# Kernel tuning notes

Hardware: AMD Instinct MI355X
Metric: run time of the kernel (lower is better)

The kernel has to match this reference:

```python
import jax, jax.numpy as jnp
import numpy as np

NUM_USER = 20000
NUM_ITEM = 20000
N = NUM_USER + NUM_ITEM
E = 250000
DIM_X = 64
NEG_SLOPE = 0.01  # F.leaky_relu default
EPS = 1e-12


def _xavier(key, shape):
    scale = (2.0 / (shape[0] + shape[1])) ** 0.5
    return jax.random.normal(key, shape, dtype=jnp.float32) * scale


def setup_inputs() -> dict:
    key = jax.random.key(0)
    ks = iter(jax.random.split(key, 64))
    inp = {}
    feat_dims = {'v': 2048, 'a': 128, 't': 100}
    lat_dims = {'v': 256, 'a': 128, 't': 100}
    for m in ('v', 'a', 't'):
        Fd, L = feat_dims[m], lat_dims[m]
        inp[m + '_feat'] = jax.random.normal(next(ks), (NUM_ITEM, Fd), dtype=jnp.float32)
        inp[m + '_pref'] = _xavier(next(ks), (NUM_USER, L))
        inp[m + '_mlp_w'] = _xavier(next(ks), (Fd, L))
        inp[m + '_mlp_b'] = jnp.zeros((L,), jnp.float32)
        inp[m + '_conv_w'] = _xavier(next(ks), (L, L))
        inp[m + '_conv_b'] = jnp.zeros((L,), jnp.float32)
        inp[m + '_lin_w'] = _xavier(next(ks), (L, DIM_X))
        inp[m + '_lin_b'] = jnp.zeros((DIM_X,), jnp.float32)
        inp[m + '_g_w'] = _xavier(next(ks), (L, DIM_X))
        inp[m + '_g_b'] = jnp.zeros((DIM_X,), jnp.float32)
    inp['id_emb'] = _xavier(next(ks), (N, DIM_X))
    src = jax.random.randint(next(ks), (E,), 0, NUM_USER)
    dst = jax.random.randint(next(ks), (E,), NUM_USER, N)
    inp['edge_index'] = jnp.stack([src, dst])  # [2, E] user->item
    inp['user_nodes'] = jax.random.randint(next(ks), (1024,), 0, NUM_USER)
    inp['pos_items'] = jax.random.randint(next(ks), (1024,), NUM_USER, N)
    inp['neg_items'] = jax.random.randint(next(ks), (1024,), NUM_USER, N)
    return inp


def _l2norm(x):
    return x / jnp.maximum(jnp.linalg.norm(x, axis=-1, keepdims=True), EPS)


def _graph_gat(x, src, dst, w, b):
    # x: [N, L] -> per-edge gather, gated attention, scatter-add (aggr='add')
    xw = x @ w                      # [N, L]
    x_j = xw[src]                   # source (neighbor) features, [E, L]
    x_i = xw[dst]                   # destination features, [E, L]
    inner = jnp.sum(x_i * x_j, axis=-1)                      # [E]
    deg = jax.ops.segment_sum(jnp.ones_like(inner), src, num_segments=N)
    gate = jax.nn.sigmoid(inner * (deg[src] ** -0.5))        # degree-scaled gate
    logits = inner * gate
    seg_max = jax.ops.segment_max(logits, dst, num_segments=N)
    e = jnp.exp(logits - seg_max[dst])
    denom = jax.ops.segment_sum(e, dst, num_segments=N)
    alpha = e / jnp.maximum(denom[dst], 1e-16)               # softmax over in-edges of dst
    out = jax.ops.segment_sum(x_j * alpha[:, None], dst, num_segments=N)
    return _l2norm(out + b)


def _gnn(feat, pref, mlp_w, mlp_b, conv_w, conv_b, lin_w, lin_b, g_w, g_b, id_emb, src, dst):
    temp = jnp.tanh(feat @ mlp_w + mlp_b)                    # [num_item, L]
    x = _l2norm(jnp.concatenate([pref, temp], axis=0))        # [N, L]
    h = jax.nn.leaky_relu(_graph_gat(x, src, dst, conv_w, conv_b), NEG_SLOPE)
    x_hat = jax.nn.leaky_relu(x @ lin_w + lin_b, NEG_SLOPE) + id_emb
    return jax.nn.leaky_relu(h @ g_w + g_b + x_hat, NEG_SLOPE)  # [N, 64]


def reference(v_feat, a_feat, t_feat,
              v_pref, v_mlp_w, v_mlp_b, v_conv_w, v_conv_b, v_lin_w, v_lin_b, v_g_w, v_g_b,
              a_pref, a_mlp_w, a_mlp_b, a_conv_w, a_conv_b, a_lin_w, a_lin_b, a_g_w, a_g_b,
              t_pref, t_mlp_w, t_mlp_b, t_conv_w, t_conv_b, t_lin_w, t_lin_b, t_g_w, t_g_b,
              id_emb, edge_index, user_nodes, pos_items, neg_items):
    # __init__ doubles the edge list with its reverse (undirected graph)
    ei = jnp.concatenate([edge_index, edge_index[::-1]], axis=1)
    src, dst = ei[0], ei[1]
    v_rep = _gnn(v_feat, v_pref, v_mlp_w, v_mlp_b, v_conv_w, v_conv_b, v_lin_w, v_lin_b, v_g_w, v_g_b, id_emb, src, dst)
    a_rep = _gnn(a_feat, a_pref, a_mlp_w, a_mlp_b, a_conv_w, a_conv_b, a_lin_w, a_lin_b, a_g_w, a_g_b, id_emb, src, dst)
    t_rep = _gnn(t_feat, t_pref, t_mlp_w, t_mlp_b, t_conv_w, t_conv_b, t_lin_w, t_lin_b, t_g_w, t_g_b, id_emb, src, dst)
    rep = (v_rep + a_rep + t_rep) / 3.0                      # [N, 64]
    pos_scores = jnp.sum(rep[user_nodes] * rep[pos_items], axis=1)
    neg_scores = jnp.sum(rep[user_nodes] * rep[neg_items], axis=1)
    return (pos_scores, neg_scores)
```

## Files before the change

### kernel.cpp

```cpp
#include <hip/hip_runtime.h>
#include <math.h>

#define NUSER 20000
#define NITEM 20000
#define NNODE 40000
#define MP_USER 20096
#define MP_NODE 40064

typedef unsigned short u16;
typedef __attribute__((ext_vector_type(8))) short bf16x8;
typedef __attribute__((ext_vector_type(4))) float f32x4;

__device__ __forceinline__ float leaky(float v){ return v > 0.0f ? v : 0.01f*v; }
__device__ __forceinline__ u16 f2bf(float f){
  unsigned u = __float_as_uint(f);
  return (u16)((u + 0x7FFFu + ((u>>16)&1u)) >> 16);
}
__device__ __forceinline__ float bf2f(u16 h){ return __uint_as_float(((unsigned)h)<<16); }
__device__ __forceinline__ unsigned pack2(u16 a, u16 b){ return (unsigned)a | ((unsigned)b<<16); }

enum { EPI_STORE=0, EPI_TANH=1, EPI_LEAKY_ADD=2, EPI_ACCUM=3, EPI_NONE=4 };

template<int WR, int WC, int MI, int EPI, bool ASPLIT, int SPLITK>
__global__ __launch_bounds__(WR*WC*64)
void wgemm_k(const float* __restrict__ A, const u16* __restrict__ Ah, const u16* __restrict__ Al,
             const u16* __restrict__ Bh, const u16* __restrict__ Bl,
             const float* __restrict__ bias, const float* __restrict__ add,
             float* __restrict__ C, int M, int N, int K, int Kp)
{
  constexpr int BM = WR*MI*16, BN = WC*64, T = WR*WC*64, NI = 4;
  __shared__ u16 Ash[4*BM*8], Asl[4*BM*8], Bsh[4*BN*8], Bsl[4*BN*8];
  const int tid = threadIdx.x, lane = tid & 63, wid = tid >> 6;
  const int wrow = wid / WC, wcol = wid % WC;
  const int row0 = blockIdx.y*BM;
  const int fr = lane & 15, kg = lane >> 4;
  const int Kc = Kp / SPLITK;
  const int ks0 = (SPLITK > 1) ? blockIdx.z * Kc : 0;

  f32x4 acc[MI][NI] = {};

  for (int kt = 0; kt < Kc; kt += 32) {
    if (ASPLIT) {
      constexpr int AG = BM*4;
      #pragma unroll
      for (int i = 0; i < 2*AG/T; i++) {
        int g = tid + i*T;
        int gi = (g < AG) ? g : g - AG;
        int r = gi >> 2, kk = gi & 3;
        size_t ofs = (size_t)(row0+r)*Kp + ks0 + kt + kk*8;
        int G = (kk*BM + (r ^ (kk<<1)))*8;
        if (g < AG) *(uint4*)&Ash[G] = *(const uint4*)(Ah + ofs);
        else        *(uint4*)&Asl[G] = *(const uint4*)(Al + ofs);
      }
    } else {
      constexpr int AG = BM*4;
      #pragma unroll
      for (int i = 0; i < AG/T; i++) {
        int g = tid + i*T;
        int r = g >> 2, kk = g & 3;
        int gr = row0 + r, gk = ks0 + kt + kk*8;
        float fv[8];
        if (gr < M && gk + 8 <= K) {
          *(float4*)&fv[0] = *(const float4*)(A + (size_t)gr*K + gk);
          *(float4*)&fv[4] = *(const float4*)(A + (size_t)gr*K + gk + 4);
        } else {
          #pragma unroll
          for (int j=0;j<8;j++) fv[j] = (gr < M && gk + j < K) ? A[(size_t)gr*K + gk + j] : 0.f;
        }
        u16 hs[8], ls[8];
        #pragma unroll
        for (int j=0;j<8;j++){ u16 h = f2bf(fv[j]); hs[j]=h; ls[j]=f2bf(fv[j]-bf2f(h)); }
        int G = (kk*BM + (r ^ (kk<<1)))*8;
        *(uint4*)&Ash[G] = make_uint4(pack2(hs[0],hs[1]),pack2(hs[2],hs[3]),pack2(hs[4],hs[5]),pack2(hs[6],hs[7]));
        *(uint4*)&Asl[G] = make_uint4(pack2(ls[0],ls[1]),pack2(ls[2],ls[3]),pack2(ls[4],ls[5]),pack2(ls[6],ls[7]));
      }
    }
    {
      constexpr int BG = BN*4;
      #pragma unroll
      for (int i = 0; i < 2*BG/T; i++) {
        int g = tid + i*T;
        int gi = (g < BG) ? g : g - BG;
        int r = gi >> 2, kk = gi & 3;
        size_t ofs = (size_t)r*Kp + ks0 + kt + kk*8;
        int G = (kk*BN + (r ^ (kk<<1)))*8;
        if (g < BG) *(uint4*)&Bsh[G] = *(const uint4*)(Bh + ofs);
        else        *(uint4*)&Bsl[G] = *(const uint4*)(Bl + ofs);
      }
    }
    __syncthreads();
    bf16x8 ah_[MI], al_[MI], bh_[NI], bl_[NI];
    #pragma unroll
    for (int mi=0;mi<MI;mi++){
      int rw = wrow*(MI*16) + mi*16 + fr;
      int G = (kg*BM + (rw ^ (kg<<1)))*8;
      ah_[mi] = *(const bf16x8*)&Ash[G];
      al_[mi] = *(const bf16x8*)&Asl[G];
    }
    #pragma unroll
    for (int ni=0;ni<NI;ni++){
      int cw = wcol*64 + ni*16 + fr;
      int G = (kg*BN + (cw ^ (kg<<1)))*8;
      bh_[ni] = *(const bf16x8*)&Bsh[G];
      bl_[ni] = *(const bf16x8*)&Bsl[G];
    }
    #pragma unroll
    for (int mi=0;mi<MI;mi++)
      #pragma unroll
      for (int ni=0;ni<NI;ni++){
        acc[mi][ni] = __builtin_amdgcn_mfma_f32_16x16x32_bf16(ah_[mi], bh_[ni], acc[mi][ni], 0,0,0);
        acc[mi][ni] = __builtin_amdgcn_mfma_f32_16x16x32_bf16(ah_[mi], bl_[ni], acc[mi][ni], 0,0,0);
        acc[mi][ni] = __builtin_amdgcn_mfma_f32_16x16x32_bf16(al_[mi], bh_[ni], acc[mi][ni], 0,0,0);
      }
    __syncthreads();
  }
  float* Cb = (EPI==EPI_NONE) ? (C + (size_t)blockIdx.z*MP_USER*N) : C;
  #pragma unroll
  for (int mi=0;mi<MI;mi++){
    #pragma unroll
    for (int ni=0;ni<NI;ni++){
      int col = wcol*64 + ni*16 + fr;
      if (EPI!=EPI_NONE && col >= N) continue;
      #pragma unroll
      for (int r=0;r<4;r++){
        int row = row0 + wrow*(MI*16) + mi*16 + kg*4 + r;
        if (EPI!=EPI_NONE && row >= M) continue;
        size_t idx = (size_t)row*N + col;
        float v = acc[mi][ni][r];
        if (EPI==EPI_NONE)           Cb[idx] = v;
        else if (EPI==EPI_STORE)     Cb[idx] = v;
        else if (EPI==EPI_TANH)      Cb[idx] = tanhf(v + bias[col]);
        else if (EPI==EPI_LEAKY_ADD) Cb[idx] = leaky(v + bias[col]) + add[idx];
        else                         Cb[idx] += leaky(v + bias[col] + add[idx]);
      }
    }
  }
}

struct WDesc { const float* w; u16 *th, *tl; int K, N, Kp, Np; };
struct WPack { WDesc d[12]; };
__global__ void split_w_k(WPack P)
{
  WDesc D = P.d[blockIdx.y];
  int gid = blockIdx.x*256 + threadIdx.x;
  int tot = D.Np * D.Kp;
  if (gid >= tot) return;
  int k = gid / D.Np, n = gid % D.Np;
  float v = (k < D.K && n < D.N) ? D.w[(size_t)k*D.N + n] : 0.f;
  u16 h = f2bf(v);
  D.th[(size_t)n*D.Kp + k] = h;
  D.tl[(size_t)n*D.Kp + k] = f2bf(v - bf2f(h));
}

__global__ void count_deg(const int* __restrict__ ei, int* __restrict__ deg, int E)
{
  int e = blockIdx.x*blockDim.x + threadIdx.x;
  if (e >= 2*E) return;
  int dst = (e < E) ? ei[e+E] : ei[e-E];
  atomicAdd(&deg[dst], 1);
}

__global__ void scan_rowptr(const int* __restrict__ deg, int* __restrict__ row_ptr, int n)
{
  __shared__ int wsum[4];
  __shared__ int carry;
  int tid = threadIdx.x, lane = tid & 63, wid = tid >> 6;
  if (tid==0) carry = 0;
  __syncthreads();
  for (int base=0; base<n; base+=1024) {
    int i0 = base + tid*4;
    int d[4];
    #pragma unroll
    for (int k=0;k<4;k++) d[k] = (i0+k < n) ? deg[i0+k] : 0;
    int t = d[0]+d[1]+d[2]+d[3];
    int incl = t;
    #pragma unroll
    for (int o=1;o<64;o<<=1){ int v = __shfl_up(incl, o); if (lane >= o) incl += v; }
    if (lane==63) wsum[wid] = incl;
    __syncthreads();
    int pre = carry;
    for (int w=0; w<wid; w++) pre += wsum[w];
    int run = pre + incl - t;
    #pragma unroll
    for (int k=0;k<4;k++){ run += d[k]; if (i0+k < n) row_ptr[i0+k+1] = run; }
    __syncthreads();
    if (tid==0) carry += wsum[0]+wsum[1]+wsum[2]+wsum[3];
  }
  if (tid==0) row_ptr[0] = 0;
}

__global__ void fill_csr(const int* __restrict__ ei, const int* __restrict__ row_ptr,
                         int* __restrict__ row_fill, int* __restrict__ col_src,
                         int* __restrict__ col_dst, int E)
{
  int e = blockIdx.x*blockDim.x + threadIdx.x;
  if (e >= 2*E) return;
  int src = ei[e];
  int dst = (e < E) ? ei[e+E] : ei[e-E];
  int pos = row_ptr[dst] + atomicAdd(&row_fill[dst], 1);
  col_src[pos] = src;
  col_dst[pos] = dst;
}

template<int VW>
__device__ __forceinline__ void loadrow(const float* __restrict__ r, int c0, int L, float* v){
  if (c0 + VW <= L) {
    if (VW==4) *(float4*)v = *(const float4*)r;
    else       *(float2*)v = *(const float2*)r;
  } else {
    #pragma unroll
    for (int j=0;j<VW;j++) v[j] = (c0+j < L) ? r[j] : 0.f;
  }
}

template<int VW>
__global__ __launch_bounds__(256)
void l2norm_split_k(const float* __restrict__ pref, const float* __restrict__ xp0,
                    const float* __restrict__ xp1, const float* __restrict__ bias,
                    u16* __restrict__ xh, u16* __restrict__ xl, int L, int Kp)
{
  int row = (blockIdx.x*blockDim.x + threadIdx.x) >> 6;
  int lane = threadIdx.x & 63;
  if (row >= MP_NODE) return;
  int c0 = lane*VW;
  size_t ofs = (size_t)row*Kp + c0;
  if (row >= NNODE) {
    if (VW==4) { *(uint2*)&xh[ofs] = make_uint2(0,0); *(uint2*)&xl[ofs] = make_uint2(0,0); }
    else       { *(unsigned*)&xh[ofs] = 0; *(unsigned*)&xl[ofs] = 0; }
    return;
  }
  float v[VW];
  if (row < NUSER) {
    loadrow<VW>(pref + (size_t)row*L + c0, c0, L, v);
  } else {
    int i = row - NUSER;
    float a[VW], b[VW];
    size_t po = (size_t)i*Kp + c0;
    if (VW==4) *(float4*)a = *(const float4*)(xp0 + po);
    else       *(float2*)a = *(const float2*)(xp0 + po);
    if (xp1) { if (VW==4) *(float4*)b = *(const float4*)(xp1 + po);
               else       *(float2*)b = *(const float2*)(xp1 + po); }
    #pragma unroll
    for (int j=0;j<VW;j++){
      int c = c0+j;
      float s = a[j] + (xp1 ? b[j] : 0.f) + ((c<L) ? bias[c] : 0.f);
      v[j] = (c<L) ? tanhf(s) : 0.f;
    }
  }
  float ss = 0.f;
  #pragma unroll
  for (int j=0;j<VW;j++) ss += v[j]*v[j];
  #pragma unroll
  for (int o=32;o;o>>=1) ss += __shfl_xor(ss, o);
  float inv = 1.0f / fmaxf(sqrtf(ss), 1e-12f);
  u16 hs[VW], ls[VW];
  #pragma unroll
  for (int j=0;j<VW;j++){
    float val = (c0+j < L) ? v[j]*inv : 0.f;
    hs[j] = f2bf(val); ls[j] = f2bf(val - bf2f(hs[j]));
  }
  if (VW==4) { *(uint2*)&xh[ofs] = make_uint2(pack2(hs[0],hs[1]),pack2(hs[2],hs[3]));
               *(uint2*)&xl[ofs] = make_uint2(pack2(ls[0],ls[1]),pack2(ls[2],ls[3])); }
  else       { *(unsigned*)&xh[ofs] = pack2(hs[0],hs[1]); *(unsigned*)&xl[ofs] = pack2(ls[0],ls[1]); }
}

__global__ __launch_bounds__(256)
void edge_logits_k(const float* __restrict__ xw, const int* __restrict__ col_src,
                   const int* __restrict__ col_dst, const int* __restrict__ deg,
                   float* __restrict__ logits, int L, int E2)
{
  int p = (blockIdx.x*blockDim.x + threadIdx.x) >> 4;
  int j = threadIdx.x & 15;
  if (p >= E2) return;
  int src = col_src[p], dst = col_dst[p];
  const float* ps = xw + (size_t)src*L;
  const float* pd = xw + (size_t)dst*L;
  float dot = 0.f;
  for (int c = j*4; c < L; c += 64) {
    float4 a = *(const float4*)(ps + c);
    float4 b = *(const float4*)(pd + c);
    dot += a.x*b.x + a.y*b.y + a.z*b.z + a.w*b.w;
  }
  #pragma unroll
  for (int o=8;o;o>>=1) dot += __shfl_xor(dot, o, 16);
  if (j==0) {
    float t = dot / sqrtf((float)deg[src]);
    float gate = 1.0f/(1.0f + expf(-t));
    logits[p] = dot * gate;
  }
}

__global__ __launch_bounds__(256)
void node_softmax(const float* __restrict__ logits, const int* __restrict__ row_ptr,
                  float* __restrict__ alpha, int n)
{
  int node = (blockIdx.x*blockDim.x + threadIdx.x) >> 6;
  int lane = threadIdx.x & 63;
  if (node >= n) return;
  int s = row_ptr[node], e = row_ptr[node+1];
  int cnt = e - s;
  if (cnt == 0) return;
  if (cnt <= 64) {
    float lv = (lane < cnt) ? logits[s+lane] : -INFINITY;
    float m = lv;
    #pragma unroll
    for (int o=32;o;o>>=1) m = fmaxf(m, __shfl_xor(m, o));
    float el = (lane < cnt) ? expf(lv - m) : 0.f;
    float d = el;
    #pragma unroll
    for (int o=32;o;o>>=1) d += __shfl_xor(d, o);
    if (lane < cnt) alpha[s+lane] = el / fmaxf(d, 1e-16f);
  } else {
    float m = -INFINITY;
    for (int q=s+lane;q<e;q+=64) m = fmaxf(m, logits[q]);
    #pragma unroll
    for (int o=32;o;o>>=1) m = fmaxf(m, __shfl_xor(m, o));
    float d = 0.f;
    for (int q=s+lane;q<e;q+=64) d += expf(logits[q]-m);
    #pragma unroll
    for (int o=32;o;o>>=1) d += __shfl_xor(d, o);
    float inv = 1.0f / fmaxf(d, 1e-16f);
    for (int q=s+lane;q<e;q+=64) alpha[q] = expf(logits[q]-m)*inv;
  }
}

template<int VW>
__global__ __launch_bounds__(256)
void aggregate_k(const float* __restrict__ xw, const float* __restrict__ alpha,
                 const int* __restrict__ row_ptr, const int* __restrict__ col_src,
                 const float* __restrict__ bias, u16* __restrict__ hh, u16* __restrict__ hl,
                 int L, int Kp)
{
  int node = (blockIdx.x*blockDim.x + threadIdx.x) >> 6;
  int lane = threadIdx.x & 63;
  if (node >= MP_NODE) return;
  int c0 = lane*VW;
  size_t ofs = (size_t)node*Kp + c0;
  if (node >= NNODE) {
    if (VW==4) { *(uint2*)&hh[ofs] = make_uint2(0,0); *(uint2*)&hl[ofs] = make_uint2(0,0); }
    else       { *(unsigned*)&hh[ofs] = 0; *(unsigned*)&hl[ofs] = 0; }
    return;
  }
  float acc[VW] = {};
  int s = row_ptr[node], e = row_ptr[node+1];
  for (int p=s;p<e;p++) {
    float a = alpha[p];
    float v[VW];
    loadrow<VW>(xw + (size_t)col_src[p]*L + c0, c0, L, v);
    #pragma unroll
    for (int j=0;j<VW;j++) acc[j] = fmaf(a, v[j], acc[j]);
  }
  float t[VW], ss = 0.f;
  #pragma unroll
  for (int j=0;j<VW;j++){ int c = c0+j; t[j] = (c<L) ? acc[j]+bias[c] : 0.f; ss += t[j]*t[j]; }
  #pragma unroll
  for (int o=32;o;o>>=1) ss += __shfl_xor(ss, o);
  float inv = 1.0f / fmaxf(sqrtf(ss), 1e-12f);
  u16 hs[VW], ls[VW];
  #pragma unroll
  for (int j=0;j<VW;j++){
    float o2 = (c0+j < L) ? leaky(t[j]*inv) : 0.f;
    hs[j] = f2bf(o2); ls[j] = f2bf(o2 - bf2f(hs[j]));
  }
  if (VW==4) { *(uint2*)&hh[ofs] = make_uint2(pack2(hs[0],hs[1]),pack2(hs[2],hs[3]));
               *(uint2*)&hl[ofs] = make_uint2(pack2(ls[0],ls[1]),pack2(ls[2],ls[3])); }
  else       { *(unsigned*)&hh[ofs] = pack2(hs[0],hs[1]); *(unsigned*)&hl[ofs] = pack2(ls[0],ls[1]); }
}

__global__ __launch_bounds__(256)
void score_k(const float* __restrict__ rep, const int* __restrict__ un,
             const int* __restrict__ pi, const int* __restrict__ ni, float* __restrict__ out)
{
  int wid = (blockIdx.x*blockDim.x + threadIdx.x) >> 6;
  int lane = threadIdx.x & 63;
  if (wid >= 2048) return;
  int i = wid & 1023;
  int isneg = wid >> 10;
  int u = un[i];
  int it = isneg ? ni[i] : pi[i];
  float p = rep[(size_t)u*64 + lane] * rep[(size_t)it*64 + lane];
  #pragma unroll
  for (int o=32;o;o>>=1) p += __shfl_xor(p, o);
  if (lane==0) out[isneg*1024 + i] = p * (1.0f/9.0f);
}

static inline size_t align_up(size_t v){ return (v + 255) & ~(size_t)255; }
static inline int cdiv(int a, int b){ return (a + b - 1) / b; }

extern "C" void kernel_launch(void* const* d_in, const int* in_sizes, int n_in,
                              void* d_out, int out_size, void* d_ws, size_t ws_size,
                              hipStream_t stream)
{
  const int E  = in_sizes[31] / 2;
  const int E2 = 2*E;

  char* p = (char*)d_ws;
  auto carve = [&](size_t bytes){ char* r = p; p += align_up(bytes); return r; };
  float* xw     = (float*)carve((size_t)NNODE*256*4);
  float* xp     = (float*)carve((size_t)2*MP_USER*256*4);
  u16*   xh     = (u16*)carve((size_t)MP_NODE*256*2);
  u16*   xl     = (u16*)carve((size_t)MP_NODE*256*2);
  float* xhat   = (float*)carve((size_t)NNODE*64*4);
  float* rep    = (float*)carve((size_t)NNODE*64*4);
  float* logits = (float*)carve((size_t)E2*4);
  float* alpha  = (float*)carve((size_t)E2*4);
  int* deg      = (int*)carve((size_t)NNODE*4);
  int* row_ptr  = (int*)carve((size_t)(NNODE+1)*4);
  int* row_fill = (int*)carve((size_t)NNODE*4);
  int* col_src  = (int*)carve((size_t)E2*4);
  int* col_dst  = (int*)carve((size_t)E2*4);

  const int* ei = (const int*)d_in[31];
  const float* id_emb = (const float*)d_in[30];

  struct Mod { const float *feat,*pref,*mlp_w,*mlp_b,*conv_w,*conv_b,*lin_w,*lin_b,*g_w,*g_b;
               int Fd, L, Kpx, Kpf, NpL; };
  Mod md[3];
  for (int m=0;m<3;m++) {
    int b = m*10;
    md[m].feat   = (const float*)d_in[b+0];
    md[m].pref   = (const float*)d_in[b+1];
    md[m].mlp_w  = (const float*)d_in[b+2];
    md[m].mlp_b  = (const float*)d_in[b+3];
    md[m].conv_w = (const float*)d_in[b+4];
    md[m].conv_b = (const float*)d_in[b+5];
    md[m].lin_w  = (const float*)d_in[b+6];
    md[m].lin_b  = (const float*)d_in[b+7];
    md[m].g_w    = (const float*)d_in[b+8];
    md[m].g_b    = (const float*)d_in[b+9];
  }
  md[0].Fd=2048; md[0].L=256; md[0].Kpx=256; md[0].Kpf=2048; md[0].NpL=256;
  md[1].Fd=128;  md[1].L=128; md[1].Kpx=128; md[1].Kpf=128;  md[1].NpL=128;
  md[2].Fd=100;  md[2].L=100; md[2].Kpx=128; md[2].Kpf=128;  md[2].NpL=128;

  u16 *wmh[3],*wml[3],*wch[3],*wcl[3],*wlh[3],*wll[3],*wgh[3],*wgl[3];
  WPack P;
  int maxTot = 0;
  for (int m=0;m<3;m++) {
    const Mod& M_ = md[m];
    size_t smlp = (size_t)M_.NpL*M_.Kpf*2, sconv = (size_t)M_.NpL*M_.Kpx*2, slin = (size_t)64*M_.Kpx*2;
    wmh[m]=(u16*)carve(smlp); wml[m]=(u16*)carve(smlp);
    wch[m]=(u16*)carve(sconv); wcl[m]=(u16*)carve(sconv);
    wlh[m]=(u16*)carve(slin);  wll[m]=(u16*)carve(slin);
    wgh[m]=(u16*)carve(slin);  wgl[m]=(u16*)carve(slin);
    P.d[m*4+0] = { M_.mlp_w,  wmh[m], wml[m], M_.Fd, M_.L, M_.Kpf, M_.NpL };
    P.d[m*4+1] = { M_.conv_w, wch[m], wcl[m], M_.L,  M_.L, M_.Kpx, M_.NpL };
    P.d[m*4+2] = { M_.lin_w,  wlh[m], wll[m], M_.L,  64,   M_.Kpx, 64 };
    P.d[m*4+3] = { M_.g_w,    wgh[m], wgl[m], M_.L,  64,   M_.Kpx, 64 };
    for (int q=0;q<4;q++){ int t = P.d[m*4+q].Np*P.d[m*4+q].Kp; if (t>maxTot) maxTot=t; }
  }

  hipMemsetAsync(deg, 0, (size_t)NNODE*4, stream);
  hipMemsetAsync(row_fill, 0, (size_t)NNODE*4, stream);
  hipMemsetAsync(rep, 0, (size_t)NNODE*64*4, stream);

  { dim3 g(cdiv(maxTot,256), 12); split_w_k<<<g,256,0,stream>>>(P); }
  {
    int blocks = cdiv(E2, 256);
    count_deg<<<blocks,256,0,stream>>>(ei, deg, E);
    scan_rowptr<<<1,256,0,stream>>>(deg, row_ptr, NNODE);
    fill_csr<<<blocks,256,0,stream>>>(ei, row_ptr, row_fill, col_src, col_dst, E);
  }

  for (int m=0;m<3;m++) {
    const Mod& M_ = md[m];
    const int L = M_.L;

    if (m == 0)
      wgemm_k<1,4,4,EPI_NONE,false,2><<<dim3(1,MP_USER/64,2),256,0,stream>>>(
          M_.feat, nullptr, nullptr, wmh[m], wml[m], nullptr, nullptr,
          xp, NUSER, 256, M_.Fd, M_.Kpf);
    else
      wgemm_k<1,2,4,EPI_NONE,false,1><<<dim3(1,MP_USER/64,1),128,0,stream>>>(
          M_.feat, nullptr, nullptr, wmh[m], wml[m], nullptr, nullptr,
          xp, NUSER, 128, M_.Fd, M_.Kpf);

    {
      const float* xp1 = (m==0) ? (xp + (size_t)MP_USER*256) : nullptr;
      if (M_.Kpx==256) l2norm_split_k<4><<<MP_NODE/4,256,0,stream>>>(M_.pref, xp, xp1, M_.mlp_b, xh, xl, L, M_.Kpx);
      else             l2norm_split_k<2><<<MP_NODE/4,256,0,stream>>>(M_.pref, xp, xp1, M_.mlp_b, xh, xl, L, M_.Kpx);
    }

    if (m == 0)
      wgemm_k<1,4,4,EPI_STORE,true,1><<<dim3(1,MP_NODE/64,1),256,0,stream>>>(
          nullptr, xh, xl, wch[m], wcl[m], nullptr, nullptr, xw, NNODE, L, L, M_.Kpx);
    else
      wgemm_k<1,2,4,EPI_STORE,true,1><<<dim3(1,MP_NODE/64,1),128,0,stream>>>(
          nullptr, xh, xl, wch[m], wcl[m], nullptr, nullptr, xw, NNODE, L, L, M_.Kpx);

    wgemm_k<4,1,2,EPI_LEAKY_ADD,true,1><<<dim3(1,MP_NODE/128,1),256,0,stream>>>(
        nullptr, xh, xl, wlh[m], wll[m], M_.lin_b, id_emb, xhat, NNODE, 64, L, M_.Kpx);

    edge_logits_k<<<cdiv(E2*16,256),256,0,stream>>>(xw, col_src, col_dst, deg, logits, L, E2);
    node_softmax<<<cdiv(NNODE*64,256),256,0,stream>>>(logits, row_ptr, alpha, NNODE);
    if (M_.Kpx==256) aggregate_k<4><<<MP_NODE/4,256,0,stream>>>(xw, alpha, row_ptr, col_src, M_.conv_b, xh, xl, L, M_.Kpx);
    else             aggregate_k<2><<<MP_NODE/4,256,0,stream>>>(xw, alpha, row_ptr, col_src, M_.conv_b, xh, xl, L, M_.Kpx);

    wgemm_k<4,1,2,EPI_ACCUM,true,1><<<dim3(1,MP_NODE/128,1),256,0,stream>>>(
        nullptr, xh, xl, wgh[m], wgl[m], M_.g_b, xhat, rep, NNODE, 64, L, M_.Kpx);
  }

  score_k<<<cdiv(2048*64,256),256,0,stream>>>(rep, (const int*)d_in[32], (const int*)d_in[33],
                                              (const int*)d_in[34], (float*)d_out);
}
```

Measured before the change: 1.180 ms.

## Register-prefetch next GEMM tile and raise split-K to four for visual MLP

The GEMM kernel now loads the next K-tile from global memory into registers while the current tile is computed, then writes it to shared memory at the top of the next iteration. This hides part of the global-load latency. The visual-modality feature GEMM (K=2048) moves from split-K 2 to 4 to expose more blocks. The l2norm kernel now sums a variable number of partial chunks, and the partial buffer is aliased onto the xw buffer to save workspace. The costs are higher register pressure from the prefetch buffers, which may reduce occupancy, and extra partial-sum traffic.

```diff
diff --git a/kernel.cpp b/kernel.cpp
--- a/kernel.cpp
+++ b/kernel.cpp
@@ -29,6 +29,10 @@
              float* __restrict__ C, int M, int N, int K, int Kp)
 {
   constexpr int BM = WR*MI*16, BN = WC*64, T = WR*WC*64, NI = 4;
+  constexpr int AG = BM*4, BG = BN*4;
+  constexpr int AITF = AG/T;
+  constexpr int AITS = 2*AG/T;
+  constexpr int BIT  = 2*BG/T;
   __shared__ u16 Ash[4*BM*8], Asl[4*BM*8], Bsh[4*BN*8], Bsl[4*BN*8];
   const int tid = threadIdx.x, lane = tid & 63, wid = tid >> 6;
   const int wrow = wid / WC, wcol = wid % WC;
@@ -39,56 +43,85 @@
 
   f32x4 acc[MI][NI] = {};
 
-  for (int kt = 0; kt < Kc; kt += 32) {
+  float fA[ASPLIT ? 1 : AITF][8];
+  uint4 uA[ASPLIT ? AITS : 1];
+  uint4 uB[BIT];
+
+  auto load_tile = [&](int kt) {
     if (ASPLIT) {
-      constexpr int AG = BM*4;
-      #pragma unroll
-      for (int i = 0; i < 2*AG/T; i++) {
+      #pragma unroll
+      for (int i = 0; i < AITS; i++) {
         int g = tid + i*T;
         int gi = (g < AG) ? g : g - AG;
         int r = gi >> 2, kk = gi & 3;
         size_t ofs = (size_t)(row0+r)*Kp + ks0 + kt + kk*8;
-        int G = (kk*BM + (r ^ (kk<<1)))*8;
-        if (g < AG) *(uint4*)&Ash[G] = *(const uint4*)(Ah + ofs);
-        else        *(uint4*)&Asl[G] = *(const uint4*)(Al + ofs);
+        uA[i] = (g < AG) ? *(const uint4*)(Ah + ofs) : *(const uint4*)(Al + ofs);
       }
     } else {
-      constexpr int AG = BM*4;
-      #pragma unroll
-      for (int i = 0; i < AG/T; i++) {
+      #pragma unroll
+      for (int i = 0; i < AITF; i++) {
         int g = tid + i*T;
         int r = g >> 2, kk = g & 3;
         int gr = row0 + r, gk = ks0 + kt + kk*8;
-        float fv[8];
         if (gr < M && gk + 8 <= K) {
-          *(float4*)&fv[0] = *(const float4*)(A + (size_t)gr*K + gk);
-          *(float4*)&fv[4] = *(const float4*)(A + (size_t)gr*K + gk + 4);
+          *(float4*)&fA[i][0] = *(const float4*)(A + (size_t)gr*K + gk);
+          *(float4*)&fA[i][4] = *(const float4*)(A + (size_t)gr*K + gk + 4);
         } else {
           #pragma unroll
-          for (int j=0;j<8;j++) fv[j] = (gr < M && gk + j < K) ? A[(size_t)gr*K + gk + j] : 0.f;
+          for (int j=0;j<8;j++) fA[i][j] = (gr < M && gk + j < K) ? A[(size_t)gr*K + gk + j] : 0.f;
         }
+      }
+    }
+    #pragma unroll
+    for (int i = 0; i < BIT; i++) {
+      int g = tid + i*T;
+      int gi = (g < BG) ? g : g - BG;
+      int r = gi >> 2, kk = gi & 3;
+      size_t ofs = (size_t)r*Kp + ks0 + kt + kk*8;
+      uB[i] = (g < BG) ? *(const uint4*)(Bh + ofs) : *(const uint4*)(Bl + ofs);
+    }
+  };
+
+  auto store_tile = [&]() {
+    if (ASPLIT) {
+      #pragma unroll
+      for (int i = 0; i < AITS; i++) {
+        int g = tid + i*T;
+        int gi = (g < AG) ? g : g - AG;
+        int r = gi >> 2, kk = gi & 3;
+        int G = (kk*BM + (r ^ (kk<<1)))*8;
+        if (g < AG) *(uint4*)&Ash[G] = uA[i];
+        else        *(uint4*)&Asl[G] = uA[i];
+      }
+    } else {
+      #pragma unroll
+      for (int i = 0; i < AITF; i++) {
+        int g = tid + i*T;
+        int r = g >> 2, kk = g & 3;
         u16 hs[8], ls[8];
         #pragma unroll
-        for (int j=0;j<8;j++){ u16 h = f2bf(fv[j]); hs[j]=h; ls[j]=f2bf(fv[j]-bf2f(h)); }
+        for (int j=0;j<8;j++){ u16 h = f2bf(fA[i][j]); hs[j]=h; ls[j]=f2bf(fA[i][j]-bf2f(h)); }
         int G = (kk*BM + (r ^ (kk<<1)))*8;
         *(uint4*)&Ash[G] = make_uint4(pack2(hs[0],hs[1]),pack2(hs[2],hs[3]),pack2(hs[4],hs[5]),pack2(hs[6],hs[7]));
         *(uint4*)&Asl[G] = make_uint4(pack2(ls[0],ls[1]),pack2(ls[2],ls[3]),pack2(ls[4],ls[5]),pack2(ls[6],ls[7]));
       }
     }
-    {
-      constexpr int BG = BN*4;
-      #pragma unroll
-      for (int i = 0; i < 2*BG/T; i++) {
-        int g = tid + i*T;
-        int gi = (g < BG) ? g : g - BG;
-        int r = gi >> 2, kk = gi & 3;
-        size_t ofs = (size_t)r*Kp + ks0 + kt + kk*8;
-        int G = (kk*BN + (r ^ (kk<<1)))*8;
-        if (g < BG) *(uint4*)&Bsh[G] = *(const uint4*)(Bh + ofs);
-        else        *(uint4*)&Bsl[G] = *(const uint4*)(Bl + ofs);
-      }
-    }
+    #pragma unroll
+    for (int i = 0; i < BIT; i++) {
+      int g = tid + i*T;
+      int gi = (g < BG) ? g : g - BG;
+      int r = gi >> 2, kk = gi & 3;
+      int G = (kk*BN + (r ^ (kk<<1)))*8;
+      if (g < BG) *(uint4*)&Bsh[G] = uB[i];
+      else        *(uint4*)&Bsl[G] = uB[i];
+    }
+  };
+
+  load_tile(0);
+  for (int kt = 0; kt < Kc; kt += 32) {
+    store_tile();
     __syncthreads();
+    if (kt + 32 < Kc) load_tile(kt + 32);
     bf16x8 ah_[MI], al_[MI], bh_[NI], bl_[NI];
     #pragma unroll
     for (int mi=0;mi<MI;mi++){
@@ -215,9 +248,9 @@
 
 template<int VW>
 __global__ __launch_bounds__(256)
-void l2norm_split_k(const float* __restrict__ pref, const float* __restrict__ xp0,
-                    const float* __restrict__ xp1, const float* __restrict__ bias,
-                    u16* __restrict__ xh, u16* __restrict__ xl, int L, int Kp)
+void l2norm_split_k(const float* __restrict__ pref, const float* __restrict__ xp,
+                    const float* __restrict__ bias,
+                    u16* __restrict__ xh, u16* __restrict__ xl, int L, int Kp, int nchunk)
 {
   int row = (blockIdx.x*blockDim.x + threadIdx.x) >> 6;
   int lane = threadIdx.x & 63;
@@ -234,17 +267,21 @@
     loadrow<VW>(pref + (size_t)row*L + c0, c0, L, v);
   } else {
     int i = row - NUSER;
-    float a[VW], b[VW];
     size_t po = (size_t)i*Kp + c0;
-    if (VW==4) *(float4*)a = *(const float4*)(xp0 + po);
-    else       *(float2*)a = *(const float2*)(xp0 + po);
-    if (xp1) { if (VW==4) *(float4*)b = *(const float4*)(xp1 + po);
-               else       *(float2*)b = *(const float2*)(xp1 + po); }
+    float s[VW] = {};
+    for (int z = 0; z < nchunk; z++) {
+      float a[VW];
+      const float* src = xp + (size_t)z*MP_USER*Kp + po;
+      if (VW==4) *(float4*)a = *(const float4*)src;
+      else       *(float2*)a = *(const float2*)src;
+      #pragma unroll
+      for (int j=0;j<VW;j++) s[j] += a[j];
+    }
     #pragma unroll
     for (int j=0;j<VW;j++){
       int c = c0+j;
-      float s = a[j] + (xp1 ? b[j] : 0.f) + ((c<L) ? bias[c] : 0.f);
-      v[j] = (c<L) ? tanhf(s) : 0.f;
+      float t = s[j] + ((c<L) ? bias[c] : 0.f);
+      v[j] = (c<L) ? tanhf(t) : 0.f;
     }
   }
   float ss = 0.f;
@@ -396,8 +433,8 @@
 
   char* p = (char*)d_ws;
   auto carve = [&](size_t bytes){ char* r = p; p += align_up(bytes); return r; };
-  float* xw     = (float*)carve((size_t)NNODE*256*4);
-  float* xp     = (float*)carve((size_t)2*MP_USER*256*4);
+  float* xw     = (float*)carve((size_t)4*MP_USER*256*4);
+  float* xp     = xw;
   u16*   xh     = (u16*)carve((size_t)MP_NODE*256*2);
   u16*   xl     = (u16*)carve((size_t)MP_NODE*256*2);
   float* xhat   = (float*)carve((size_t)NNODE*64*4);
@@ -467,7 +504,7 @@
     const int L = M_.L;
 
     if (m == 0)
-      wgemm_k<1,4,4,EPI_NONE,false,2><<<dim3(1,MP_USER/64,2),256,0,stream>>>(
+      wgemm_k<1,4,4,EPI_NONE,false,4><<<dim3(1,MP_USER/64,4),256,0,stream>>>(
           M_.feat, nullptr, nullptr, wmh[m], wml[m], nullptr, nullptr,
           xp, NUSER, 256, M_.Fd, M_.Kpf);
     else
@@ -476,9 +513,9 @@
           xp, NUSER, 128, M_.Fd, M_.Kpf);
 
     {
-      const float* xp1 = (m==0) ? (xp + (size_t)MP_USER*256) : nullptr;
-      if (M_.Kpx==256) l2norm_split_k<4><<<MP_NODE/4,256,0,stream>>>(M_.pref, xp, xp1, M_.mlp_b, xh, xl, L, M_.Kpx);
-      else             l2norm_split_k<2><<<MP_NODE/4,256,0,stream>>>(M_.pref, xp, xp1, M_.mlp_b, xh, xl, L, M_.Kpx);
+      int nchunk = (m==0) ? 4 : 1;
+      if (M_.Kpx==256) l2norm_split_k<4><<<MP_NODE/4,256,0,stream>>>(M_.pref, xp, M_.mlp_b, xh, xl, L, M_.Kpx, nchunk);
+      else             l2norm_split_k<2><<<MP_NODE/4,256,0,stream>>>(M_.pref, xp, M_.mlp_b, xh, xl, L, M_.Kpx, nchunk);
     }
 
     if (m == 0)
```

New measurement: 1.482 ms. 25.6% more time.
